# Optimization experiments

Measured on AMD Instinct MI355X. Metric: run time of the kernel, lower is better.

## Reference

```python
import jax, jax.numpy as jnp
import numpy as np

INPUT_DIM, DIM_K, DIM_V = 1024, 512, 512

def setup_inputs() -> dict:
    key = jax.random.key(0)
    kx, kq, kk, kv = jax.random.split(key, 4)
    x = jax.random.normal(kx, (4, 4096, INPUT_DIM), dtype=jnp.float32)
    s = 1.0 / np.sqrt(INPUT_DIM)
    Wq = jax.random.normal(kq, (INPUT_DIM, DIM_K), dtype=jnp.float32) * s
    Wk = jax.random.normal(kk, (INPUT_DIM, DIM_K), dtype=jnp.float32) * s
    Wv = jax.random.normal(kv, (INPUT_DIM, DIM_V), dtype=jnp.float32) * s
    return {"x": x, "Wq": Wq, "Wk": Wk, "Wv": Wv}

def reference(x, Wq, Wk, Wv):
    # x: [b, n, d_in]; bias-free projections
    Q = jnp.einsum('bnd,dk->bnk', x, Wq)
    K = jnp.einsum('bnd,dk->bnk', x, Wk)
    V = jnp.einsum('bnd,dv->bnv', x, Wv)
    scale = 1.0 / np.sqrt(Wq.shape[1])
    scores = jnp.einsum('bqk,bnk->bqn', Q, K) * scale  # [b, n, n]
    atten = jax.nn.softmax(scores, axis=-1)
    return jnp.einsum('bqn,bnv->bqv', atten, V)
```

## Files before the change

kernel.cpp:

```cpp
#include <hip/hip_runtime.h>
#include <hip/hip_bf16.h>


typedef __attribute__((ext_vector_type(8))) short bf16x8;
typedef __attribute__((ext_vector_type(4))) float floatx4;

static __device__ __forceinline__ unsigned short f2bf(float f) {
    unsigned int u = __builtin_bit_cast(unsigned int, f);
    return (unsigned short)((u + 0x7fffu + ((u >> 16) & 1u)) >> 16);
}

static __device__ __forceinline__ void gl2lds16(const unsigned short* g, unsigned short* l) {
    __builtin_amdgcn_global_load_lds(
        (const __attribute__((address_space(1))) unsigned int*)g,
        (__attribute__((address_space(3))) unsigned int*)l, 16, 0, 0);
}

#define BAR() __asm__ volatile("s_barrier" ::: "memory")
#define WVMC12() __asm__ volatile("s_waitcnt vmcnt(12)" ::: "memory")
#define WVMC8() __asm__ volatile("s_waitcnt vmcnt(8)" ::: "memory")
#define WLGKM0() __asm__ volatile("s_waitcnt lgkmcnt(0)" ::: "memory")
#define WALL() __asm__ volatile("s_waitcnt vmcnt(0) lgkmcnt(0)" ::: "memory")

__global__ __launch_bounds__(256) void cvt_bf16(const float* __restrict__ X,
                                                unsigned short* __restrict__ Y, int n4) {
    int i = blockIdx.x * 256 + threadIdx.x;
    if (i < n4) {
        float4 v = reinterpret_cast<const float4*>(X)[i];
        ushort4 o;
        o.x = f2bf(v.x); o.y = f2bf(v.y); o.z = f2bf(v.z); o.w = f2bf(v.w);
        reinterpret_cast<ushort4*>(Y)[i] = o;
    }
}

__global__ __launch_bounds__(256) void transpose_w(const float* __restrict__ W,
                                                   unsigned short* __restrict__ Wt, int off) {
    __shared__ float tile[32][33];
    int n0 = blockIdx.x * 32;
    int k0 = blockIdx.y * 32;
    int tx = threadIdx.x & 31, ty = threadIdx.x >> 5;
    for (int i = 0; i < 32; i += 8)
        tile[ty + i][tx] = W[(size_t)(k0 + ty + i) * 512 + n0 + tx];
    __syncthreads();
    for (int i = 0; i < 32; i += 8)
        Wt[(size_t)(off + n0 + ty + i) * 1024 + k0 + tx] = f2bf(tile[tx][ty + i]);
}

__global__ __launch_bounds__(256) void gemm_qkv(const unsigned short* __restrict__ A,
                                                const unsigned short* __restrict__ Bt,
                                                unsigned short* __restrict__ Qb,
                                                unsigned short* __restrict__ Kfr,
                                                unsigned short* __restrict__ Vfr) {
    __shared__ unsigned short As[128 * 32];
    __shared__ unsigned short Bs[128 * 32];
    const int K = 1024;
    const int m0 = blockIdx.y * 128, n0 = blockIdx.x * 128;
    const int tid = threadIdx.x;
    const int lane = tid & 63, wave = tid >> 6;
    const int wm = (wave >> 1) * 64, wn = (wave & 1) * 64;
    const int quad = lane >> 4, l15 = lane & 15;

    floatx4 acc[4][4] = {};
    const int srow = tid >> 2, scol = (tid & 3) * 8;

    for (int kt = 0; kt < K; kt += 32) {
        const unsigned short* ga = A + (size_t)(m0 + srow) * K + kt + scol;
        const unsigned short* gb = Bt + (size_t)(n0 + srow) * K + kt + scol;
        gl2lds16(ga, As + tid * 8);
        gl2lds16(ga + (size_t)64 * K, As + 2048 + tid * 8);
        gl2lds16(gb, Bs + tid * 8);
        gl2lds16(gb + (size_t)64 * K, Bs + 2048 + tid * 8);
        __syncthreads();
        bf16x8 af[4], bfr[4];
#pragma unroll
        for (int i = 0; i < 4; i++)
            af[i] = *reinterpret_cast<const bf16x8*>(As + (wm + i * 16 + l15) * 32 + quad * 8);
#pragma unroll
        for (int j = 0; j < 4; j++)
            bfr[j] = *reinterpret_cast<const bf16x8*>(Bs + (wn + j * 16 + l15) * 32 + quad * 8);
#pragma unroll
        for (int i = 0; i < 4; i++)
#pragma unroll
            for (int j = 0; j < 4; j++)
                acc[i][j] = __builtin_amdgcn_mfma_f32_16x16x32_bf16(af[i], bfr[j], acc[i][j], 0, 0, 0);
        __syncthreads();
    }

    const float qscale = 0.044194173824159216f;
#pragma unroll
    for (int i = 0; i < 4; i++)
#pragma unroll
        for (int j = 0; j < 4; j++)
#pragma unroll
            for (int r = 0; r < 4; r++) {
                int row = m0 + wm + i * 16 + quad * 4 + r;
                int col = n0 + wn + j * 16 + l15;
                if (n0 < 512) {
                    Qb[(size_t)row * 512 + col] = f2bf(acc[i][j][r] * qscale);
                } else if (n0 < 1024) {
                    int d = col - 512;
                    size_t base = ((size_t)((row >> 12) * 128 + ((row & 4095) >> 5))) << 14;
                    int off = ((d >> 5) * 2 + ((row >> 4) & 1)) * 512 +
                              (((d >> 3) & 3) * 16 + (row & 15)) * 8 + (d & 7);
                    Kfr[base + off] = f2bf(acc[i][j][r]);
                } else {
                    int d = col - 1024;
                    size_t base = ((size_t)((row >> 12) * 128 + ((row & 4095) >> 5))) << 14;
                    int off = (d >> 4) * 512 +
                              (((row & 31) >> 3) * 16 + (d & 15)) * 8 + (row & 7);
                    Vfr[base + off] = f2bf(acc[i][j][r]);
                }
            }
}

__global__ __launch_bounds__(512, 2) void attn(const unsigned short* __restrict__ Qg,
                                               const unsigned short* __restrict__ Kf,
                                               const unsigned short* __restrict__ Vf,
                                               float* __restrict__ O0,
                                               float* __restrict__ O1,
                                               float* __restrict__ lpart) {
    __shared__ unsigned short Kb[2][16384];
    __shared__ unsigned short Vb[2][16384];
    __shared__ unsigned short Ps[8][512];

    const int L = blockIdx.x;
    const int b = L & 3;
    const int h = (L >> 2) & 1;
    const int q0 = (L >> 3) * 128;
    const int tid = threadIdx.x;
    const int lane = tid & 63, wave = tid >> 6;
    const int quad = lane >> 4, l15 = lane & 15;
    const int qh = wave >> 2, dq = wave & 3;

    const unsigned short* KfB = Kf + ((size_t)b << 21);
    const unsigned short* VfB = Vf + ((size_t)b << 21);
    float* Od = (h == 0) ? O0 : O1;

    bf16x8 qf[16];
    {
        const unsigned short* qrow =
            Qg + (size_t)(b * 4096 + q0 + wave * 16 + l15) * 512 + quad * 8;
#pragma unroll
        for (int ks = 0; ks < 16; ks++)
            qf[ks] = *reinterpret_cast<const bf16x8*>(qrow + ks * 32);
    }
    WALL();

    floatx4 o[4][8];
#pragma unroll
    for (int g = 0; g < 4; g++)
#pragma unroll
        for (int n2 = 0; n2 < 8; n2++) o[g][n2] = floatx4{0.f, 0.f, 0.f, 0.f};
    float lp = 0.f;

    const int kt0 = h * 64;
    {
        const unsigned short* gK = KfB + ((size_t)kt0 << 14);
        const unsigned short* gV = VfB + ((size_t)kt0 << 14);
#pragma unroll
        for (int i = 0; i < 4; i++)
            gl2lds16(gK + (i * 512 + tid) * 8, &Kb[0][(i * 512 + tid) * 8]);
#pragma unroll
        for (int i = 0; i < 4; i++)
            gl2lds16(gV + (i * 512 + tid) * 8, &Vb[0][(i * 512 + tid) * 8]);
    }

    for (int it = 0; it < 64; it++) {
        const int cur = it & 1, nxt = cur ^ 1;
        const int ktn = kt0 + ((it + 1) & 63);
        {
            const unsigned short* gK = KfB + ((size_t)ktn << 14);
            const unsigned short* gV = VfB + ((size_t)ktn << 14);
#pragma unroll
            for (int i = 0; i < 4; i++)
                gl2lds16(gK + (i * 512 + tid) * 8, &Kb[nxt][(i * 512 + tid) * 8]);
#pragma unroll
            for (int i = 0; i < 4; i++)
                gl2lds16(gV + (i * 512 + tid) * 8, &Vb[nxt][(i * 512 + tid) * 8]);
        }
        WVMC12();
        BAR();

        const unsigned short* Kc = &Kb[cur][0];
        floatx4 s00 = {0.f,0.f,0.f,0.f}, s01 = {0.f,0.f,0.f,0.f};
        floatx4 s10 = {0.f,0.f,0.f,0.f}, s11 = {0.f,0.f,0.f,0.f};
#pragma unroll
        for (int ks = 0; ks < 16; ks += 2) {
            bf16x8 k0a = *reinterpret_cast<const bf16x8*>(Kc + (2 * ks + 0) * 512 + lane * 8);
            bf16x8 k1a = *reinterpret_cast<const bf16x8*>(Kc + (2 * ks + 1) * 512 + lane * 8);
            bf16x8 k0b = *reinterpret_cast<const bf16x8*>(Kc + (2 * ks + 2) * 512 + lane * 8);
            bf16x8 k1b = *reinterpret_cast<const bf16x8*>(Kc + (2 * ks + 3) * 512 + lane * 8);
            s00 = __builtin_amdgcn_mfma_f32_16x16x32_bf16(k0a, qf[ks], s00, 0, 0, 0);
            s10 = __builtin_amdgcn_mfma_f32_16x16x32_bf16(k1a, qf[ks], s10, 0, 0, 0);
            s01 = __builtin_amdgcn_mfma_f32_16x16x32_bf16(k0b, qf[ks + 1], s01, 0, 0, 0);
            s11 = __builtin_amdgcn_mfma_f32_16x16x32_bf16(k1b, qf[ks + 1], s11, 0, 0, 0);
        }
        floatx4 s0v = s00 + s01, s1v = s10 + s11;

        {
            float p0[4], p1[4];
#pragma unroll
            for (int r = 0; r < 4; r++) {
                p0[r] = __expf(s0v[r] - 16.0f);
                p1[r] = __expf(s1v[r] - 16.0f);
                lp += p0[r] + p1[r];
            }
            unsigned int a0, a1, b0, b1;
            asm("v_cvt_pk_bf16_f32 %0, %1, %2" : "=v"(a0) : "v"(p0[0]), "v"(p0[1]));
            asm("v_cvt_pk_bf16_f32 %0, %1, %2" : "=v"(a1) : "v"(p0[2]), "v"(p0[3]));
            asm("v_cvt_pk_bf16_f32 %0, %1, %2" : "=v"(b0) : "v"(p1[0]), "v"(p1[1]));
            asm("v_cvt_pk_bf16_f32 %0, %1, %2" : "=v"(b1) : "v"(p1[2]), "v"(p1[3]));
            unsigned short* Pw = &Ps[wave][0];
            const int wo = (quad >> 1) * 128 + l15 * 8 + (quad & 1) * 4;
            *reinterpret_cast<uint2*>(Pw + wo)       = uint2{a0, a1};
            *reinterpret_cast<uint2*>(Pw + wo + 256) = uint2{b0, b1};
        }
        WLGKM0();
        WVMC8();
        BAR();

        const unsigned short* Vc = &Vb[cur][0];
        bf16x8 vfr[8];
#pragma unroll
        for (int n2 = 0; n2 < 8; n2++)
            vfr[n2] = *reinterpret_cast<const bf16x8*>(Vc + (dq * 8 + n2) * 512 + lane * 8);
#pragma unroll
        for (int g = 0; g < 4; g++) {
            bf16x8 pf = *reinterpret_cast<const bf16x8*>(&Ps[qh * 4 + g][0] + lane * 8);
#pragma unroll
            for (int n2 = 0; n2 < 8; n2++)
                o[g][n2] = __builtin_amdgcn_mfma_f32_16x16x32_bf16(pf, vfr[n2], o[g][n2], 0, 0, 0);
        }
        BAR();
    }
    WALL();

    lp += __shfl_xor(lp, 16);
    lp += __shfl_xor(lp, 32);
    if (quad == 0)
        lpart[h * 16384 + b * 4096 + q0 + wave * 16 + l15] = lp;

#pragma unroll
    for (int g = 0; g < 4; g++)
#pragma unroll
        for (int r = 0; r < 4; r++) {
            size_t rowoff = (size_t)(b * 4096 + q0 + qh * 64 + g * 16 + quad * 4 + r) * 512
                            + dq * 128 + l15;
#pragma unroll
            for (int n2 = 0; n2 < 8; n2++)
                Od[rowoff + n2 * 16] = o[g][n2][r];
        }
}

__global__ __launch_bounds__(256) void combine(float* __restrict__ Out,
                                               const float* __restrict__ O1,
                                               const float* __restrict__ lpart) {
    int i = blockIdx.x * 256 + threadIdx.x;
    int row = i >> 7;
    float inv = 1.0f / (lpart[row] + lpart[16384 + row]);
    float4 a = reinterpret_cast<const float4*>(Out)[i];
    float4 c = reinterpret_cast<const float4*>(O1)[i];
    float4 r;
    r.x = (a.x + c.x) * inv;
    r.y = (a.y + c.y) * inv;
    r.z = (a.z + c.z) * inv;
    r.w = (a.w + c.w) * inv;
    reinterpret_cast<float4*>(Out)[i] = r;
}

extern "C" void kernel_launch(void* const* d_in, const int* in_sizes, int n_in,
                              void* d_out, int out_size, void* d_ws, size_t ws_size,
                              hipStream_t stream) {
    const float* x  = (const float*)d_in[0];
    const float* Wq = (const float*)d_in[1];
    const float* Wk = (const float*)d_in[2];
    const float* Wv = (const float*)d_in[3];

    char* ws = (char*)d_ws;
    unsigned short* Wtall = (unsigned short*)(ws);
    unsigned short* Qb  = (unsigned short*)(ws + (3u << 20));
    unsigned short* Kfr = (unsigned short*)(ws + (19u << 20));
    unsigned short* Vfr = (unsigned short*)(ws + (35u << 20));
    unsigned short* xb  = (unsigned short*)(ws + (51u << 20));
    float* O1    = (float*)(ws + (51u << 20));
    float* lpart = (float*)(ws + (83u << 20));

    dim3 tb(256);
    cvt_bf16<<<dim3(16384), tb, 0, stream>>>(x, xb, 16384 * 1024 / 4);
    transpose_w<<<dim3(16, 32), tb, 0, stream>>>(Wq, Wtall, 0);
    transpose_w<<<dim3(16, 32), tb, 0, stream>>>(Wk, Wtall, 512);
    transpose_w<<<dim3(16, 32), tb, 0, stream>>>(Wv, Wtall, 1024);
    gemm_qkv<<<dim3(12, 128), tb, 0, stream>>>(xb, Wtall, Qb, Kfr, Vfr);
    attn<<<dim3(256), dim3(512), 0, stream>>>(Qb, Kfr, Vfr, (float*)d_out, O1, lpart);
    combine<<<dim3(8192), tb, 0, stream>>>((float*)d_out, O1, lpart);
}
```

Baseline: 360.0 us.

## Restructure attention K/V prefetch with triple-buffered V and remap GEMM block order

In the attention kernel, the single double-buffered K+V prefetch becomes two staggered streams. K sits in one buffer and is reloaded right after the second barrier. V uses a three-slot ring that is loaded at the start of each iteration, and P is double-buffered, so the trailing barrier per iteration can be removed. The QK and PV MFMA loops are also wrapped in s_setprio raises to favour matrix issue. The QKV GEMM switches to a 1D grid with a swizzled tile order, likely to improve L2 reuse of the A/B tiles. The trade-off is less prefetch lead time for K, since its load is issued only during the PV phase, and a larger LDS footprint for the extra V slot.

```diff
diff --git a/kernel.cpp b/kernel.cpp
--- a/kernel.cpp
+++ b/kernel.cpp
@@ -17,8 +17,8 @@
 }
 
 #define BAR() __asm__ volatile("s_barrier" ::: "memory")
-#define WVMC12() __asm__ volatile("s_waitcnt vmcnt(12)" ::: "memory")
-#define WVMC8() __asm__ volatile("s_waitcnt vmcnt(8)" ::: "memory")
+#define WVMC4() __asm__ volatile("s_waitcnt vmcnt(4)" ::: "memory")
+#define WVMC0() __asm__ volatile("s_waitcnt vmcnt(0)" ::: "memory")
 #define WLGKM0() __asm__ volatile("s_waitcnt lgkmcnt(0)" ::: "memory")
 #define WALL() __asm__ volatile("s_waitcnt vmcnt(0) lgkmcnt(0)" ::: "memory")
 
@@ -54,7 +54,10 @@
     __shared__ unsigned short As[128 * 32];
     __shared__ unsigned short Bs[128 * 32];
     const int K = 1024;
-    const int m0 = blockIdx.y * 128, n0 = blockIdx.x * 128;
+    const int L = blockIdx.x;
+    const int mt = ((L & 7) << 4) | ((L >> 3) & 15);
+    const int nt = L >> 7;
+    const int m0 = mt * 128, n0 = nt * 128;
     const int tid = threadIdx.x;
     const int lane = tid & 63, wave = tid >> 6;
     const int wm = (wave >> 1) * 64, wn = (wave & 1) * 64;
@@ -119,9 +122,9 @@
                                                float* __restrict__ O0,
                                                float* __restrict__ O1,
                                                float* __restrict__ lpart) {
-    __shared__ unsigned short Kb[2][16384];
-    __shared__ unsigned short Vb[2][16384];
-    __shared__ unsigned short Ps[8][512];
+    __shared__ unsigned short Kb[16384];
+    __shared__ unsigned short Vb[3][16384];
+    __shared__ unsigned short Ps[2][8][512];
 
     const int L = blockIdx.x;
     const int b = L & 3;
@@ -156,34 +159,26 @@
     const int kt0 = h * 64;
     {
         const unsigned short* gK = KfB + ((size_t)kt0 << 14);
-        const unsigned short* gV = VfB + ((size_t)kt0 << 14);
 #pragma unroll
         for (int i = 0; i < 4; i++)
-            gl2lds16(gK + (i * 512 + tid) * 8, &Kb[0][(i * 512 + tid) * 8]);
-#pragma unroll
-        for (int i = 0; i < 4; i++)
-            gl2lds16(gV + (i * 512 + tid) * 8, &Vb[0][(i * 512 + tid) * 8]);
-    }
-
+            gl2lds16(gK + (i * 512 + tid) * 8, &Kb[(i * 512 + tid) * 8]);
+    }
+
+    int vs = 0;
     for (int it = 0; it < 64; it++) {
-        const int cur = it & 1, nxt = cur ^ 1;
-        const int ktn = kt0 + ((it + 1) & 63);
         {
-            const unsigned short* gK = KfB + ((size_t)ktn << 14);
-            const unsigned short* gV = VfB + ((size_t)ktn << 14);
+            const unsigned short* gV = VfB + ((size_t)(kt0 + it) << 14);
 #pragma unroll
             for (int i = 0; i < 4; i++)
-                gl2lds16(gK + (i * 512 + tid) * 8, &Kb[nxt][(i * 512 + tid) * 8]);
-#pragma unroll
-            for (int i = 0; i < 4; i++)
-                gl2lds16(gV + (i * 512 + tid) * 8, &Vb[nxt][(i * 512 + tid) * 8]);
-        }
-        WVMC12();
+                gl2lds16(gV + (i * 512 + tid) * 8, &Vb[vs][(i * 512 + tid) * 8]);
+        }
+        WVMC4();
         BAR();
 
-        const unsigned short* Kc = &Kb[cur][0];
+        const unsigned short* Kc = &Kb[0];
         floatx4 s00 = {0.f,0.f,0.f,0.f}, s01 = {0.f,0.f,0.f,0.f};
         floatx4 s10 = {0.f,0.f,0.f,0.f}, s11 = {0.f,0.f,0.f,0.f};
+        __builtin_amdgcn_s_setprio(1);
 #pragma unroll
         for (int ks = 0; ks < 16; ks += 2) {
             bf16x8 k0a = *reinterpret_cast<const bf16x8*>(Kc + (2 * ks + 0) * 512 + lane * 8);
@@ -195,6 +190,7 @@
             s01 = __builtin_amdgcn_mfma_f32_16x16x32_bf16(k0b, qf[ks + 1], s01, 0, 0, 0);
             s11 = __builtin_amdgcn_mfma_f32_16x16x32_bf16(k1b, qf[ks + 1], s11, 0, 0, 0);
         }
+        __builtin_amdgcn_s_setprio(0);
         floatx4 s0v = s00 + s01, s1v = s10 + s11;
 
         {
@@ -210,28 +206,38 @@
             asm("v_cvt_pk_bf16_f32 %0, %1, %2" : "=v"(a1) : "v"(p0[2]), "v"(p0[3]));
             asm("v_cvt_pk_bf16_f32 %0, %1, %2" : "=v"(b0) : "v"(p1[0]), "v"(p1[1]));
             asm("v_cvt_pk_bf16_f32 %0, %1, %2" : "=v"(b1) : "v"(p1[2]), "v"(p1[3]));
-            unsigned short* Pw = &Ps[wave][0];
+            unsigned short* Pw = &Ps[it & 1][wave][0];
             const int wo = (quad >> 1) * 128 + l15 * 8 + (quad & 1) * 4;
             *reinterpret_cast<uint2*>(Pw + wo)       = uint2{a0, a1};
             *reinterpret_cast<uint2*>(Pw + wo + 256) = uint2{b0, b1};
         }
         WLGKM0();
-        WVMC8();
+        WVMC0();
         BAR();
 
-        const unsigned short* Vc = &Vb[cur][0];
+        {
+            const unsigned short* gK = KfB + ((size_t)(kt0 + ((it + 1) & 63)) << 14);
+#pragma unroll
+            for (int i = 0; i < 4; i++)
+                gl2lds16(gK + (i * 512 + tid) * 8, &Kb[(i * 512 + tid) * 8]);
+        }
+
+        const unsigned short* Vc = &Vb[vs][0];
         bf16x8 vfr[8];
 #pragma unroll
         for (int n2 = 0; n2 < 8; n2++)
             vfr[n2] = *reinterpret_cast<const bf16x8*>(Vc + (dq * 8 + n2) * 512 + lane * 8);
+        __builtin_amdgcn_s_setprio(1);
 #pragma unroll
         for (int g = 0; g < 4; g++) {
-            bf16x8 pf = *reinterpret_cast<const bf16x8*>(&Ps[qh * 4 + g][0] + lane * 8);
+            bf16x8 pf = *reinterpret_cast<const bf16x8*>(&Ps[it & 1][qh * 4 + g][0] + lane * 8);
 #pragma unroll
             for (int n2 = 0; n2 < 8; n2++)
                 o[g][n2] = __builtin_amdgcn_mfma_f32_16x16x32_bf16(pf, vfr[n2], o[g][n2], 0, 0, 0);
         }
-        BAR();
+        __builtin_amdgcn_s_setprio(0);
+
+        vs = (vs == 2) ? 0 : vs + 1;
     }
     WALL();
 
@@ -290,7 +296,7 @@
     transpose_w<<<dim3(16, 32), tb, 0, stream>>>(Wq, Wtall, 0);
     transpose_w<<<dim3(16, 32), tb, 0, stream>>>(Wk, Wtall, 512);
     transpose_w<<<dim3(16, 32), tb, 0, stream>>>(Wv, Wtall, 1024);
-    gemm_qkv<<<dim3(12, 128), tb, 0, stream>>>(xb, Wtall, Qb, Kfr, Vfr);
+    gemm_qkv<<<dim3(1536), tb, 0, stream>>>(xb, Wtall, Qb, Kfr, Vfr);
     attn<<<dim3(256), dim3(512), 0, stream>>>(Qb, Kfr, Vfr, (float*)d_out, O1, lpart);
     combine<<<dim3(8192), tb, 0, stream>>>((float*)d_out, O1, lpart);
 }
```

After: 341.3 us. 5.2% less time.
